# Performance work log

Hardware: AMD Instinct MI355X
Metric: run time of the kernel (lower is better)

## Reference

```python
import jax, jax.numpy as jnp
import numpy as np
from jax import lax

K = 9          # box kernel side
PAD = K // 2   # same padding
K_SUM = float(K * K * K)


def _box_sum(x):
    """Sliding-window sum over a 9x9x9 box, zero-padded (separable 1D convs).
    x: [B, 1, D, H, W] -> same shape."""
    dn = ('NCDHW', 'OIDHW', 'NCDHW')
    for ax in range(3):  # D, H, W
        kshape = [1, 1, 1, 1, 1]
        kshape[2 + ax] = K
        w = jnp.ones(kshape, dtype=x.dtype)
        pad = [(0, 0), (0, 0), (0, 0)]
        pad[ax] = (PAD, PAD)
        x = lax.conv_general_dilated(x, w, window_strides=(1, 1, 1),
                                     padding=pad, dimension_numbers=dn)
    return x


def setup_inputs() -> dict:
    key = jax.random.key(0)
    k1, k2 = jax.random.split(key)
    shape = (2, 1, 192, 192, 192)  # [B, 1, D, H, W]
    I = jax.random.uniform(k1, shape, dtype=jnp.float32)
    J = jax.random.uniform(k2, shape, dtype=jnp.float32)
    return {"I": I, "J": J}


def reference(I, J):
    II = I * I
    JJ = J * J
    IJ = I * J
    I_sum = _box_sum(I)
    J_sum = _box_sum(J)
    II_sum = _box_sum(II)
    JJ_sum = _box_sum(JJ)
    IJ_sum = _box_sum(IJ)
    I_u = I / K_SUM
    J_u = J / K_SUM
    cross = IJ_sum - I_sum * J_u - J_sum * I_u + I_u * J_u * K_SUM
    I_var = II_sum - 2 * I_sum * I_u + I_u * I_u * K_SUM
    J_var = JJ_sum - 2 * J_sum * J_u + J_u * J_u * K_SUM
    top = cross * cross
    bottom = I_var * J_var + 1e-5
    return -jnp.mean(top / bottom)
```

## Files before the change

kernel.cpp:

```cpp
#include <hip/hip_runtime.h>
#include <hip/hip_bf16.h>

#define WDIM 192
#define PLANE (192 * 192)
#define VOL (192 * 192 * 192)
#define HC 16
#define TR (HC + 8)
#define NCH 12
#define RWU 100
#define DC 24

typedef __fp16 h2f __attribute__((ext_vector_type(2)));
typedef unsigned int u32x2 __attribute__((ext_vector_type(2)));

static __device__ inline unsigned int pk_h16(float a, float b) {
    h2f v = __builtin_amdgcn_cvt_pkrtz(a, b);
    return __builtin_bit_cast(unsigned int, v);
}
static __device__ inline float dot2u(unsigned int a, unsigned int b, float c) {
    return __builtin_amdgcn_fdot2(__builtin_bit_cast(h2f, a),
                                  __builtin_bit_cast(h2f, b), c, false);
}

static __device__ inline unsigned int pk_bf16(float a, float b) {
    union { __hip_bfloat162 v; unsigned int u; } cvt;
    cvt.v = __float22bfloat162_rn(make_float2(a, b));
    return cvt.u;
}
static __device__ inline float bf_lo(unsigned int u) {
    union { unsigned int u; float f; } c; c.u = u << 16; return c.f;
}
static __device__ inline float bf_hi(unsigned int u) {
    union { unsigned int u; float f; } c; c.u = u & 0xffff0000u; return c.f;
}

__global__ __launch_bounds__(192) void wh_pass(const float* __restrict__ I,
                                               const float* __restrict__ J,
                                               u32x2* __restrict__ B2,
                                               unsigned int* __restrict__ B1,
                                               float* __restrict__ out0) {
    __shared__ unsigned int sI[TR * RWU];
    __shared__ unsigned int sJ[TR * RWU];
    const int t = threadIdx.x;
    const int d = blockIdx.x / NCH;
    const int c = blockIdx.x - d * NCH;
    const int h0 = c * HC;

    if (out0 && blockIdx.x == 0 && blockIdx.y == 0 && t == 0) *out0 = 0.0f;

    const size_t bofs = (size_t)blockIdx.y * VOL;
    const float* Ib = I + bofs;
    const float* Jb = J + bofs;
    u32x2* B2b = B2 + bofs;
    unsigned int* B1b = B1 + bofs;

    const size_t dbase = (size_t)d * PLANE;

    {
        const int row = t >> 3;
        const int p = t & 7;
        unsigned int* dst = (p < 4) ? sI : sJ;
        const int q = p & 3;
        const int col = (q < 2) ? q : (96 + q);
        dst[row * RWU + col] = 0u;
    }

    #pragma unroll
    for (int i = 0; i < 6; ++i) {
        const int idx4 = i * 192 + t;
        const int row  = idx4 / 48;
        const int col4 = (idx4 - row * 48) * 4;
        const int h = h0 - 4 + row;
        float4 vI = make_float4(0.f, 0.f, 0.f, 0.f);
        float4 vJ = vI;
        if (h >= 0 && h < WDIM) {
            vI = *(const float4*)(Ib + dbase + (size_t)h * WDIM + col4);
            vJ = *(const float4*)(Jb + dbase + (size_t)h * WDIM + col4);
        }
        uint2 uI, uJ;
        uI.x = pk_h16(vI.x, vI.y); uI.y = pk_h16(vI.z, vI.w);
        uJ.x = pk_h16(vJ.x, vJ.y); uJ.y = pk_h16(vJ.z, vJ.w);
        const int ui = row * RWU + 2 + (col4 >> 1);
        *(uint2*)&sI[ui] = uI;
        *(uint2*)&sJ[ui] = uJ;
    }
    __syncthreads();

    const int tb = t >> 1;
    const int odd = t & 1;
    const unsigned int ONESF = 0x3C003C00u;
    const unsigned int ones0 = odd ? 0x3C000000u : ONESF;
    const unsigned int ones4 = odd ? ONESF : 0x00003C00u;
    const unsigned int keep0 = odd ? 0xFFFF0000u : 0xFFFFFFFFu;
    const unsigned int keep4 = odd ? 0xFFFFFFFFu : 0x0000FFFFu;

    float ring0[9], ring1[9], ring2[9], ring3[9], ring4[9];
    #pragma unroll
    for (int j = 0; j < 9; ++j) { ring0[j]=0.f; ring1[j]=0.f; ring2[j]=0.f; ring3[j]=0.f; ring4[j]=0.f; }
    float s0 = 0.f, s1 = 0.f, s2 = 0.f, s3 = 0.f, s4 = 0.f;

    unsigned int AI[5], AJ[5], BI[5], BJ[5];
    #pragma unroll
    for (int p = 0; p < 5; ++p) { AI[p] = sI[tb + p]; AJ[p] = sJ[tb + p]; }

    #pragma unroll
    for (int s = 0; s < TR; ++s) {
        if (s + 1 < TR) {
            const int base = (s + 1) * RWU + tb;
            if ((s & 1) == 0) {
                #pragma unroll
                for (int p = 0; p < 5; ++p) { BI[p] = sI[base + p]; BJ[p] = sJ[base + p]; }
            } else {
                #pragma unroll
                for (int p = 0; p < 5; ++p) { AI[p] = sI[base + p]; AJ[p] = sJ[base + p]; }
            }
        }
        const unsigned int c0 = ((s & 1) == 0) ? AI[0] : BI[0];
        const unsigned int c1 = ((s & 1) == 0) ? AI[1] : BI[1];
        const unsigned int c2 = ((s & 1) == 0) ? AI[2] : BI[2];
        const unsigned int c3 = ((s & 1) == 0) ? AI[3] : BI[3];
        const unsigned int c4 = ((s & 1) == 0) ? AI[4] : BI[4];
        const unsigned int e0 = ((s & 1) == 0) ? AJ[0] : BJ[0];
        const unsigned int e1 = ((s & 1) == 0) ? AJ[1] : BJ[1];
        const unsigned int e2 = ((s & 1) == 0) ? AJ[2] : BJ[2];
        const unsigned int e3 = ((s & 1) == 0) ? AJ[3] : BJ[3];
        const unsigned int e4 = ((s & 1) == 0) ? AJ[4] : BJ[4];

        const unsigned int mI0 = c0 & keep0, mI4 = c4 & keep4;
        const unsigned int mJ0 = e0 & keep0, mJ4 = e4 & keep4;

        float w0 = dot2u(c0, ones0, 0.f);
        w0 = dot2u(c1, ONESF, w0); w0 = dot2u(c2, ONESF, w0);
        w0 = dot2u(c3, ONESF, w0); w0 = dot2u(c4, ones4, w0);

        float w1 = dot2u(e0, ones0, 0.f);
        w1 = dot2u(e1, ONESF, w1); w1 = dot2u(e2, ONESF, w1);
        w1 = dot2u(e3, ONESF, w1); w1 = dot2u(e4, ones4, w1);

        float w2 = dot2u(mI0, c0, 0.f);
        w2 = dot2u(c1, c1, w2); w2 = dot2u(c2, c2, w2);
        w2 = dot2u(c3, c3, w2); w2 = dot2u(mI4, c4, w2);

        float w3 = dot2u(mJ0, e0, 0.f);
        w3 = dot2u(e1, e1, w3); w3 = dot2u(e2, e2, w3);
        w3 = dot2u(e3, e3, w3); w3 = dot2u(mJ4, e4, w3);

        float w4 = dot2u(mI0, e0, 0.f);
        w4 = dot2u(c1, e1, w4); w4 = dot2u(c2, e2, w4);
        w4 = dot2u(c3, e3, w4); w4 = dot2u(mI4, e4, w4);

        const int j = s % 9;
        s0 += w0 - ring0[j]; ring0[j] = w0;
        s1 += w1 - ring1[j]; ring1[j] = w1;
        s2 += w2 - ring2[j]; ring2[j] = w2;
        s3 += w3 - ring3[j]; ring3[j] = w3;
        s4 += w4 - ring4[j]; ring4[j] = w4;

        if (s >= 8) {
            const int h_out = h0 + s - 8;
            const size_t idx = dbase + (size_t)h_out * WDIM + t;
            u32x2 v2; v2.x = pk_bf16(s0, s1); v2.y = pk_bf16(s2, s3);
            __builtin_nontemporal_store(v2, B2b + idx);
            __builtin_nontemporal_store(pk_bf16(s4, 0.f), B1b + idx);
        }
    }
}

__global__ __launch_bounds__(192) void d_pass(const u32x2* __restrict__ B2,
                                              const unsigned int* __restrict__ B1,
                                              const float* __restrict__ I,
                                              const float* __restrict__ J,
                                              float* __restrict__ out) {
    const int t = threadIdx.x;
    const int h = blockIdx.x >> 3;
    const int c = blockIdx.x & 7;
    const int d0 = c * DC;
    const int base_h = h * WDIM + t;

    const size_t bofs = (size_t)blockIdx.y * VOL;
    const float* Ib = I + bofs;
    const float* Jb = J + bofs;
    const u32x2* B2b = B2 + bofs;
    const unsigned int* B1b = B1 + bofs;

    float r0[9], r1[9], r2[9], r3[9], r4[9];
    #pragma unroll
    for (int j = 0; j < 9; ++j) { r0[j]=0.f; r1[j]=0.f; r2[j]=0.f; r3[j]=0.f; r4[j]=0.f; }
    float s0 = 0.f, s1 = 0.f, s2 = 0.f, s3 = 0.f, s4 = 0.f;

    const float inv_k = 1.0f / 729.0f;
    float local = 0.f;

    uint3 qA[8], qB[8];
    float2 cA[8], cB[8];
    #pragma unroll
    for (int i = 0; i < 8; ++i) {
        const int d_in = d0 - 4 + i;
        qA[i] = make_uint3(0u, 0u, 0u);
        if (d_in >= 0 && d_in < WDIM) {
            const size_t pos = (size_t)d_in * PLANE + base_h;
            const u32x2 v2 = B2b[pos];
            qA[i] = make_uint3(v2.x, v2.y, B1b[pos]);
        }
        cA[i] = make_float2(0.f, 0.f);
    }

    #pragma unroll
    for (int g = 0; g < 4; ++g) {
        if (g + 1 < 4) {
            #pragma unroll
            for (int i = 0; i < 8; ++i) {
                const int s = (g + 1) * 8 + i;
                const int d_in = d0 - 4 + s;
                uint3 v = make_uint3(0u, 0u, 0u);
                if (d_in >= 0 && d_in < WDIM) {
                    const size_t pos = (size_t)d_in * PLANE + base_h;
                    const u32x2 v2 = B2b[pos];
                    v = make_uint3(v2.x, v2.y, B1b[pos]);
                }
                const int d_out = d0 + s - 8;
                const size_t cidx = (size_t)d_out * PLANE + base_h;
                const float ci = Ib[cidx];
                const float cj = Jb[cidx];
                if ((g & 1) == 0) { qB[i] = v; cB[i] = make_float2(ci, cj); }
                else              { qA[i] = v; cA[i] = make_float2(ci, cj); }
            }
        }
        #pragma unroll
        for (int i = 0; i < 8; ++i) {
            const int s = g * 8 + i;
            const uint3 q = ((g & 1) == 0) ? qA[i] : qB[i];
            const float f0 = bf_lo(q.x), f1 = bf_hi(q.x);
            const float f2 = bf_lo(q.y), f3 = bf_hi(q.y);
            const float f4 = bf_lo(q.z);
            const int j = s % 9;
            s0 += f0 - r0[j]; r0[j] = f0;
            s1 += f1 - r1[j]; r1[j] = f1;
            s2 += f2 - r2[j]; r2[j] = f2;
            s3 += f3 - r3[j]; r3[j] = f3;
            s4 += f4 - r4[j]; r4[j] = f4;

            if (s >= 8) {
                const float2 cc = ((g & 1) == 0) ? cA[i] : cB[i];
                const float Iu = cc.x * inv_k;
                const float Ju = cc.y * inv_k;
                const float cross = s4 - s0 * Ju - s1 * Iu + Iu * Ju * 729.0f;
                const float Ivar  = s2 - 2.0f * s0 * Iu + Iu * Iu * 729.0f;
                const float Jvar  = s3 - 2.0f * s1 * Ju + Ju * Ju * 729.0f;
                local += (cross * cross) * __builtin_amdgcn_rcpf(Ivar * Jvar + 1e-5f);
            }
        }
    }

    __shared__ float sred[192];
    sred[t] = local;
    __syncthreads();
    if (t < 64) {
        float v = sred[t] + sred[t + 64] + sred[t + 128];
        #pragma unroll
        for (int off = 32; off; off >>= 1) v += __shfl_down(v, off);
        if (t == 0) {
            atomicAdd(out, v * (-1.0f / 14155776.0f));
        }
    }
}

extern "C" void kernel_launch(void* const* d_in, const int* in_sizes, int n_in,
                              void* d_out, int out_size, void* d_ws, size_t ws_size,
                              hipStream_t stream) {
    const float* I = (const float*)d_in[0];
    const float* J = (const float*)d_in[1];
    float* out = (float*)d_out;

    const size_t need2 = (size_t)2 * VOL * 12;
    if (ws_size >= need2) {
        u32x2* B2 = (u32x2*)d_ws;
        unsigned int* B1 = (unsigned int*)((char*)d_ws + (size_t)2 * VOL * 8);
        wh_pass<<<dim3(WDIM * NCH, 2), 192, 0, stream>>>(I, J, B2, B1, out);
        d_pass <<<dim3(WDIM * 8, 2), 192, 0, stream>>>(B2, B1, I, J, out);
    } else {
        u32x2* B2 = (u32x2*)d_ws;
        unsigned int* B1 = (unsigned int*)((char*)d_ws + (size_t)VOL * 8);
        for (int b = 0; b < 2; ++b) {
            const float* Ib = I + (size_t)b * VOL;
            const float* Jb = J + (size_t)b * VOL;
            wh_pass<<<dim3(WDIM * NCH, 1), 192, 0, stream>>>(Ib, Jb, B2, B1,
                                                             b == 0 ? out : nullptr);
            d_pass <<<dim3(WDIM * 8, 1), 192, 0, stream>>>(B2, B1, Ib, Jb, out);
        }
    }
}
```

Baseline: 216.1 us.

## Enlarge W/H pass row chunks, use cached stores, remap D-pass blocks for L2 locality

The W/H pass now processes 24-row chunks (8 per plane) instead of 16, which cuts the halo rows each block loads and recomputes. Its intermediate bf16 outputs are written with normal stores instead of nontemporal ones, so they can stay in cache for the D pass. The D pass block index is remapped so that consecutively scheduled blocks walk h rows matching the W/H chunking, aiming for better cache reuse of those intermediates. The risks are fewer blocks in the first pass and cache pollution from the regular stores.

```diff
diff --git a/kernel.cpp b/kernel.cpp
--- a/kernel.cpp
+++ b/kernel.cpp
@@ -4,9 +4,9 @@
 #define WDIM 192
 #define PLANE (192 * 192)
 #define VOL (192 * 192 * 192)
-#define HC 16
+#define HC 24
 #define TR (HC + 8)
-#define NCH 12
+#define NCH 8
 #define RWU 100
 #define DC 24
 
@@ -42,8 +42,8 @@
     __shared__ unsigned int sI[TR * RWU];
     __shared__ unsigned int sJ[TR * RWU];
     const int t = threadIdx.x;
-    const int d = blockIdx.x / NCH;
-    const int c = blockIdx.x - d * NCH;
+    const int d = blockIdx.x >> 3;
+    const int c = blockIdx.x & 7;
     const int h0 = c * HC;
 
     if (out0 && blockIdx.x == 0 && blockIdx.y == 0 && t == 0) *out0 = 0.0f;
@@ -56,9 +56,9 @@
 
     const size_t dbase = (size_t)d * PLANE;
 
-    {
-        const int row = t >> 3;
-        const int p = t & 7;
+    for (int n = t; n < TR * 8; n += 192) {
+        const int row = n >> 3;
+        const int p = n & 7;
         unsigned int* dst = (p < 4) ? sI : sJ;
         const int q = p & 3;
         const int col = (q < 2) ? q : (96 + q);
@@ -66,7 +66,7 @@
     }
 
     #pragma unroll
-    for (int i = 0; i < 6; ++i) {
+    for (int i = 0; i < TR * 48 / 192; ++i) {
         const int idx4 = i * 192 + t;
         const int row  = idx4 / 48;
         const int col4 = (idx4 - row * 48) * 4;
@@ -160,8 +160,8 @@
             const int h_out = h0 + s - 8;
             const size_t idx = dbase + (size_t)h_out * WDIM + t;
             u32x2 v2; v2.x = pk_bf16(s0, s1); v2.y = pk_bf16(s2, s3);
-            __builtin_nontemporal_store(v2, B2b + idx);
-            __builtin_nontemporal_store(pk_bf16(s4, 0.f), B1b + idx);
+            B2b[idx] = v2;
+            B1b[idx] = pk_bf16(s4, 0.f);
         }
     }
 }
@@ -172,8 +172,10 @@
                                               const float* __restrict__ J,
                                               float* __restrict__ out) {
     const int t = threadIdx.x;
-    const int h = blockIdx.x >> 3;
-    const int c = blockIdx.x & 7;
+    const int g = blockIdx.x & 7;
+    const int q = blockIdx.x >> 3;
+    const int h = g * HC + (q % HC);
+    const int c = q / HC;
     const int d0 = c * DC;
     const int base_h = h * WDIM + t;
 
@@ -206,11 +208,11 @@
     }
 
     #pragma unroll
-    for (int g = 0; g < 4; ++g) {
-        if (g + 1 < 4) {
+    for (int gg = 0; gg < 4; ++gg) {
+        if (gg + 1 < 4) {
             #pragma unroll
             for (int i = 0; i < 8; ++i) {
-                const int s = (g + 1) * 8 + i;
+                const int s = (gg + 1) * 8 + i;
                 const int d_in = d0 - 4 + s;
                 uint3 v = make_uint3(0u, 0u, 0u);
                 if (d_in >= 0 && d_in < WDIM) {
@@ -222,17 +224,17 @@
                 const size_t cidx = (size_t)d_out * PLANE + base_h;
                 const float ci = Ib[cidx];
                 const float cj = Jb[cidx];
-                if ((g & 1) == 0) { qB[i] = v; cB[i] = make_float2(ci, cj); }
-                else              { qA[i] = v; cA[i] = make_float2(ci, cj); }
+                if ((gg & 1) == 0) { qB[i] = v; cB[i] = make_float2(ci, cj); }
+                else               { qA[i] = v; cA[i] = make_float2(ci, cj); }
             }
         }
         #pragma unroll
         for (int i = 0; i < 8; ++i) {
-            const int s = g * 8 + i;
-            const uint3 q = ((g & 1) == 0) ? qA[i] : qB[i];
-            const float f0 = bf_lo(q.x), f1 = bf_hi(q.x);
-            const float f2 = bf_lo(q.y), f3 = bf_hi(q.y);
-            const float f4 = bf_lo(q.z);
+            const int s = gg * 8 + i;
+            const uint3 qv = ((gg & 1) == 0) ? qA[i] : qB[i];
+            const float f0 = bf_lo(qv.x), f1 = bf_hi(qv.x);
+            const float f2 = bf_lo(qv.y), f3 = bf_hi(qv.y);
+            const float f4 = bf_lo(qv.z);
             const int j = s % 9;
             s0 += f0 - r0[j]; r0[j] = f0;
             s1 += f1 - r1[j]; r1[j] = f1;
@@ -241,7 +243,7 @@
             s4 += f4 - r4[j]; r4[j] = f4;
 
             if (s >= 8) {
-                const float2 cc = ((g & 1) == 0) ? cA[i] : cB[i];
+                const float2 cc = ((gg & 1) == 0) ? cA[i] : cB[i];
                 const float Iu = cc.x * inv_k;
                 const float Ju = cc.y * inv_k;
                 const float cross = s4 - s0 * Ju - s1 * Iu + Iu * Ju * 729.0f;
```

Result: no change. 216.7 us (+0.3%).
